# Kernel tuning notes

Hardware: AMD Instinct MI355X
Metric: run time of the kernel (lower is better)

The kernel has to match this reference:

```python
import jax, jax.numpy as jnp
import numpy as np

EMBED_DIM = 1024
NUM_HEADS = 16
HEAD_DIM = EMBED_DIM // NUM_HEADS


def setup_inputs() -> dict:
    key = jax.random.key(0)
    ks = jax.random.split(key, 12)
    B, S, E = 2, 2048, EMBED_DIM
    scale = 1.0 / np.sqrt(E)
    inp = {
        "query": jax.random.normal(ks[0], (B, S, E), dtype=jnp.float32),
        "key": jax.random.normal(ks[1], (B, S, E), dtype=jnp.float32),
        "value": jax.random.normal(ks[2], (B, S, E), dtype=jnp.float32),
        "key_padding_mask": jax.random.randint(ks[3], (B, S), 0, 2).astype(bool),
        # Linear params (torch nn.Linear: y = x @ W.T + b)
        "Wq": jax.random.normal(ks[4], (E, E), dtype=jnp.float32) * scale,
        "bq": jnp.zeros((E,), dtype=jnp.float32),
        "Wk": jax.random.normal(ks[5], (E, E), dtype=jnp.float32) * scale,
        "bk": jnp.zeros((E,), dtype=jnp.float32),
        "Wv": jax.random.normal(ks[6], (E, E), dtype=jnp.float32) * scale,
        "bv": jnp.zeros((E,), dtype=jnp.float32),
        "Wo": jax.random.normal(ks[7], (E, E), dtype=jnp.float32) * scale,
        "bo": jnp.zeros((E,), dtype=jnp.float32),
    }
    return inp


def reference(query, key, value, key_padding_mask, Wq, bq, Wk, bk, Wv, bv, Wo, bo):
    B, Sq, E = query.shape
    H, D = NUM_HEADS, HEAD_DIM

    def split_heads(x, W, b):
        y = x @ W.T + b                      # [B, S, E]
        return y.reshape(B, -1, H, D).transpose(0, 2, 1, 3)  # [B, H, S, D]

    q = split_heads(query, Wq, bq)
    k = split_heads(key, Wk, bk)
    v = split_heads(value, Wv, bv)

    scores = jnp.einsum("bhqd,bhkd->bhqk", q, k) / jnp.sqrt(jnp.float32(D))
    scores = jnp.where(key_padding_mask[:, None, None, :], -jnp.inf, scores)
    probs = jax.nn.softmax(scores, axis=-1)  # dropout p=0.0 -> identity
    attn = jnp.einsum("bhqk,bhkd->bhqd", probs, v)
    attn = attn.transpose(0, 2, 1, 3).reshape(B, Sq, E)
    return attn @ Wo.T + bo
```

## Files before the change

kernel.cpp:

```cpp
#include <hip/hip_runtime.h>
#include <hip/hip_bf16.h>

#define BATCH 2
#define SEQ   2048
#define EMBED 1024
#define NHEAD 16
#define HDIM  64

typedef __bf16 bf16x8 __attribute__((ext_vector_type(8)));
typedef __bf16 bf16x4 __attribute__((ext_vector_type(4)));
typedef float  floatx4 __attribute__((ext_vector_type(4)));

struct ConvAll { const void* src[7]; void* dst[7]; unsigned n[7]; };

__device__ __forceinline__ int derive_isbf(const void* qptr) {
    const unsigned short* u = (const unsigned short*)qptr;
    int sane = 0;
    for (int k = 0; k < 64; ++k) {
        int e = (u[2 * k] >> 7) & 0xff;
        if (e >= 117 && e <= 137) sane++;
    }
    return (sane >= 40) ? 1 : 0;
}

__global__ __launch_bounds__(256) void prep_convert(
        ConvAll a, const void* qptr, const void* mptr,
        int* flags, __hip_bfloat16* mones) {
    if (blockIdx.y == 7) {
        if (blockIdx.x >= 16) return;
        const unsigned int* w = (const unsigned int*)mptr;
        int all01 = 1, allf = 1;
        for (int i = 0; i < 64; ++i) {
            unsigned int x = w[i];
            if (!(x == 0u || x == 1u)) all01 = 0;
            if (!(x == 0u || x == 0x3F800000u)) allf = 0;
        }
        const int bytemask = (all01 || allf) ? 0 : 1;
        const int i = blockIdx.x * 256 + threadIdx.x;
        int v;
        if (bytemask) v = (((const unsigned char*)mptr)[i] != 0);
        else          v = (((const unsigned int*)mptr)[i] != 0u);
        mones[i] = __float2bfloat16(v ? 0.f : 1.f);
        if (blockIdx.x == 0 && threadIdx.x == 0) {
            flags[0] = derive_isbf(qptr);
            flags[1] = bytemask;
        }
        return;
    }
    if (derive_isbf(qptr)) return;
    const int t = blockIdx.y;
    const unsigned n8 = a.n[t] / 8;
    const unsigned stride = gridDim.x * blockDim.x;
    for (unsigned i = blockIdx.x * blockDim.x + threadIdx.x; i < n8; i += stride) {
        const unsigned base = i * 8;
        const float* s = (const float*)a.src[t] + base;
        __hip_bfloat16 tmp[8];
#pragma unroll
        for (int j = 0; j < 8; ++j) tmp[j] = __float2bfloat16(s[j]);
        *(uint4*)((__hip_bfloat16*)a.dst[t] + base) = *(const uint4*)tmp;
    }
}

__device__ __forceinline__ void gload_lds16(const __hip_bfloat16* g, __bf16* l) {
    __builtin_amdgcn_global_load_lds(
        (const __attribute__((address_space(1))) unsigned int*)g,
        (__attribute__((address_space(3))) unsigned int*)l, 16, 0, 0);
}

struct GemmIO {
    const void* Xr; const __hip_bfloat16* Xc;
    const void* Wr; const __hip_bfloat16* Wc;
    const void* br;
    void* Y;
    float osc;
};
struct GemmArgs { GemmIO io[3]; };

__global__ __launch_bounds__(256, 2) void gemm_mfma(
        GemmArgs args, int M, int N, int K, const int* flags,
        const __hip_bfloat16* __restrict__ mones) {
    const GemmIO io = args.io[blockIdx.z];
    const int isbf = flags[0];
    const __hip_bfloat16* Xp = isbf ? (const __hip_bfloat16*)io.Xr : io.Xc;
    const __hip_bfloat16* Wp = isbf ? (const __hip_bfloat16*)io.Wr : io.Wc;
    __shared__ __bf16 Xs[128 * 64];
    __shared__ __bf16 Ws[128 * 64];
    const int lane = threadIdx.x & 63, wv = threadIdx.x >> 6;
    const int wr = wv >> 1, wc = wv & 1;
    const int l = lane & 15, quad = lane >> 4;

    const int lin = blockIdx.x + blockIdx.y * 8;
    const int tsw = (lin & 7) * 32 + (lin >> 3);
    const int row0 = (tsw >> 3) * 128, col0 = (tsw & 7) * 128;

    const int srow = lane >> 3;
    const int schunk = (lane & 7) ^ srow;
    const __hip_bfloat16* xbase = Xp + (size_t)(row0 + srow) * K + schunk * 8;
    const __hip_bfloat16* wbase = Wp + (size_t)(col0 + srow) * K + schunk * 8;

    floatx4 acc[4][4] = {};

    for (int k0 = 0; k0 < K; k0 += 64) {
        __syncthreads();
#pragma unroll
        for (int i = 0; i < 4; ++i) {
            const int instr = wv * 4 + i;
            gload_lds16(xbase + (size_t)instr * 8 * K + k0, &Xs[instr * 512]);
        }
#pragma unroll
        for (int i = 0; i < 4; ++i) {
            const int instr = wv * 4 + i;
            gload_lds16(wbase + (size_t)instr * 8 * K + k0, &Ws[instr * 512]);
        }
        __syncthreads();
#pragma unroll
        for (int kk = 0; kk < 2; ++kk) {
            bf16x8 af[4], bfr[4];
#pragma unroll
            for (int m = 0; m < 4; ++m)
                af[m] = *(const bf16x8*)
                    &Xs[(wr * 64 + m * 16 + l) * 64 + ((kk * 4 + quad) ^ (l & 7)) * 8];
#pragma unroll
            for (int n = 0; n < 4; ++n)
                bfr[n] = *(const bf16x8*)
                    &Ws[(wc * 64 + n * 16 + l) * 64 + ((kk * 4 + quad) ^ (l & 7)) * 8];
#pragma unroll
            for (int m = 0; m < 4; ++m)
#pragma unroll
                for (int n = 0; n < 4; ++n)
                    acc[m][n] = __builtin_amdgcn_mfma_f32_16x16x32_bf16(
                        af[m], bfr[n], acc[m][n], 0, 0, 0);
        }
    }

    if (blockIdx.z == 2) {
#pragma unroll
        for (int m = 0; m < 4; ++m) {
            const int rb = row0 + wr * 64 + m * 16 + quad * 4;
            const int b = rb >> 11, s0 = rb & (SEQ - 1);
            float mf[4];
#pragma unroll
            for (int r = 0; r < 4; ++r)
                mf[r] = __bfloat162float(mones[rb + r]);
#pragma unroll
            for (int n = 0; n < 4; ++n) {
                const int col = col0 + wc * 64 + n * 16 + l;
                const int h = col >> 6, d = col & 63;
                const float bv = isbf
                    ? __bfloat162float(((const __hip_bfloat16*)io.br)[col])
                    : ((const float*)io.br)[col];
                bf16x4 out;
#pragma unroll
                for (int r = 0; r < 4; ++r)
                    out[r] = (__bf16)((acc[m][n][r] + bv) * mf[r]);
                *(bf16x4*)((__hip_bfloat16*)io.Y +
                           ((size_t)((b << 4) + h) * HDIM + d) * SEQ + s0) = out;
            }
        }
    } else {
#pragma unroll
        for (int m = 0; m < 4; ++m) {
#pragma unroll
            for (int n = 0; n < 4; ++n) {
                const int col = col0 + wc * 64 + n * 16 + l;
                const float bv = isbf
                    ? __bfloat162float(((const __hip_bfloat16*)io.br)[col])
                    : ((const float*)io.br)[col];
#pragma unroll
                for (int r = 0; r < 4; ++r) {
                    const int row = row0 + wr * 64 + m * 16 + quad * 4 + r;
                    const float v = (acc[m][n][r] + bv) * io.osc;
                    ((__hip_bfloat16*)io.Y)[(size_t)row * N + col] = __float2bfloat16(v);
                }
            }
        }
    }
}

__global__ __launch_bounds__(256, 2) void gemm_out(
        const __hip_bfloat16* __restrict__ X,
        const void* __restrict__ Wr, const __hip_bfloat16* __restrict__ Wc,
        const void* __restrict__ bias, void* __restrict__ Y,
        const int* flags) {
    const int N = EMBED, K = EMBED;
    const int isbf = flags[0];
    const __hip_bfloat16* Wp = isbf ? (const __hip_bfloat16*)Wr : Wc;
    __shared__ __bf16 Xs[64 * 64];
    __shared__ __bf16 Ws[128 * 64];
    const int lane = threadIdx.x & 63, wv = threadIdx.x >> 6;
    const int wr = wv >> 1, wc = wv & 1;
    const int l = lane & 15, quad = lane >> 4;

    const int lin = blockIdx.x + blockIdx.y * 8;
    const int tsw = (lin & 7) * 64 + (lin >> 3);
    const int row0 = (tsw >> 3) * 64, col0 = (tsw & 7) * 128;

    const int srow = lane >> 3;
    const int schunk = (lane & 7) ^ srow;
    const __hip_bfloat16* xbase = X + (size_t)(row0 + srow) * K + schunk * 8;
    const __hip_bfloat16* wbase = Wp + (size_t)(col0 + srow) * K + schunk * 8;

    floatx4 acc[2][4] = {};

    for (int k0 = 0; k0 < K; k0 += 64) {
        __syncthreads();
#pragma unroll
        for (int i = 0; i < 2; ++i) {
            const int instr = wv * 2 + i;
            gload_lds16(xbase + (size_t)instr * 8 * K + k0, &Xs[instr * 512]);
        }
#pragma unroll
        for (int i = 0; i < 4; ++i) {
            const int instr = wv * 4 + i;
            gload_lds16(wbase + (size_t)instr * 8 * K + k0, &Ws[instr * 512]);
        }
        __syncthreads();
#pragma unroll
        for (int kk = 0; kk < 2; ++kk) {
            bf16x8 af[2], bfr[4];
#pragma unroll
            for (int m = 0; m < 2; ++m)
                af[m] = *(const bf16x8*)
                    &Xs[(wr * 32 + m * 16 + l) * 64 + ((kk * 4 + quad) ^ (l & 7)) * 8];
#pragma unroll
            for (int n = 0; n < 4; ++n)
                bfr[n] = *(const bf16x8*)
                    &Ws[(wc * 64 + n * 16 + l) * 64 + ((kk * 4 + quad) ^ (l & 7)) * 8];
#pragma unroll
            for (int m = 0; m < 2; ++m)
#pragma unroll
                for (int n = 0; n < 4; ++n)
                    acc[m][n] = __builtin_amdgcn_mfma_f32_16x16x32_bf16(
                        af[m], bfr[n], acc[m][n], 0, 0, 0);
        }
    }

#pragma unroll
    for (int m = 0; m < 2; ++m) {
#pragma unroll
        for (int n = 0; n < 4; ++n) {
            const int col = col0 + wc * 64 + n * 16 + l;
            const float bv = isbf
                ? __bfloat162float(((const __hip_bfloat16*)bias)[col])
                : ((const float*)bias)[col];
#pragma unroll
            for (int r = 0; r < 4; ++r) {
                const int row = row0 + wr * 32 + m * 16 + quad * 4 + r;
                const float v = acc[m][n][r] + bv;
                if (isbf)
                    ((__hip_bfloat16*)Y)[(size_t)row * N + col] = __float2bfloat16(v);
                else
                    ((float*)Y)[(size_t)row * N + col] = v;
            }
        }
    }
}

__global__ __launch_bounds__(512, 4) void attn_mfma(
        const __hip_bfloat16* __restrict__ Qb,
        const __hip_bfloat16* __restrict__ Kb,
        const __hip_bfloat16* __restrict__ Vt,
        const __hip_bfloat16* __restrict__ mones,
        __hip_bfloat16* __restrict__ Ao) {
    const int bh = blockIdx.x, b = bh >> 4, h = bh & 15;
    const int q0 = blockIdx.y * 128;
    const int wv = threadIdx.x >> 6, lane = threadIdx.x & 63;
    const int l = lane & 15, quad = lane >> 4;

    __shared__ __bf16 Ks[2][128 * 64];
    __shared__ __bf16 Vs[2][64 * 128];

    bf16x8 aQ[2];
    {
        const int qrow = q0 + wv * 16 + l;
        const __hip_bfloat16* qp =
            Qb + ((size_t)(b * SEQ + qrow)) * EMBED + h * HDIM + quad * 8;
        aQ[0] = *(const bf16x8*)qp;
        aQ[1] = *(const bf16x8*)(qp + 32);
    }

    floatx4 O[4] = {};
    floatx4 Ol = {};
    const int rho = 8 * (l >> 2) + (l & 3);

    const int ksrow = lane >> 3, kpc = lane & 7;
    const int vsrow = lane >> 4, vpc = lane & 15;
    const __hip_bfloat16* mbase = mones + b * SEQ;

    auto stage = [&](int k0, int buf) {
#pragma unroll
        for (int i = 0; i < 2; ++i) {
            const int row = wv * 16 + i * 8 + ksrow;
            const int sc = kpc ^ ((row & 3) | (((row >> 3) & 1) << 2));
            gload_lds16(Kb + ((size_t)(b * SEQ + k0 + row)) * EMBED + h * HDIM +
                            sc * 8,
                        &Ks[buf][(wv * 16 + i * 8) * 64]);
        }
#pragma unroll
        for (int i = 0; i < 2; ++i) {
            const int row = wv * 8 + i * 4 + vsrow;
            const int sc = vpc ^ (row & 15);
            gload_lds16(Vt + ((size_t)(bh * HDIM + row)) * SEQ + k0 + sc * 8,
                        &Vs[buf][(wv * 8 + i * 4) * 128]);
        }
    };

    auto compute = [&](int k0, int buf) {
#pragma unroll
        for (int kh2 = 0; kh2 < 2; ++kh2) {
            bf16x8 a0[4], a1[4];
#pragma unroll
            for (int n = 0; n < 4; ++n) {
                const int rr = kh2 * 64 + 32 * (n >> 1) + 4 * (n & 1) + rho;
                const int f = (rr & 3) | (((rr >> 3) & 1) << 2);
                a0[n] = *(const bf16x8*)&Ks[buf][rr * 64 + ((quad) ^ f) * 8];
                a1[n] = *(const bf16x8*)&Ks[buf][rr * 64 + ((quad + 4) ^ f) * 8];
            }
            bf16x8 bv[2][4];
#pragma unroll
            for (int kh = 0; kh < 2; ++kh)
#pragma unroll
                for (int dt = 0; dt < 4; ++dt) {
                    const int c = kh2 * 8 + kh * 4 + quad;
                    bv[kh][dt] = *(const bf16x8*)
                        &Vs[buf][(dt * 16 + l) * 128 + (c ^ l) * 8];
                }
            bf16x8 vm[2];
#pragma unroll
            for (int kh = 0; kh < 2; ++kh)
                vm[kh] = *(const bf16x8*)
                    (mbase + k0 + kh2 * 64 + kh * 32 + quad * 8);

            floatx4 S[4];
            __builtin_amdgcn_s_setprio(1);
#pragma unroll
            for (int n = 0; n < 4; ++n) {
                floatx4 c = {};
                c = __builtin_amdgcn_mfma_f32_16x16x32_bf16(a0[n], aQ[0],
                                                            c, 0, 0, 0);
                c = __builtin_amdgcn_mfma_f32_16x16x32_bf16(a1[n], aQ[1],
                                                            c, 0, 0, 0);
                S[n] = c;
            }
            __builtin_amdgcn_s_setprio(0);
#pragma unroll
            for (int n = 0; n < 4; ++n)
#pragma unroll
                for (int r = 0; r < 4; ++r)
                    S[n][r] = __builtin_amdgcn_exp2f(S[n][r]);
#pragma unroll
            for (int kh = 0; kh < 2; ++kh) {
                bf16x8 ap;
#pragma unroll
                for (int j = 0; j < 4; ++j) {
                    ap[j]     = (__bf16)S[2 * kh][j];
                    ap[j + 4] = (__bf16)S[2 * kh + 1][j];
                }
                __builtin_amdgcn_s_setprio(1);
#pragma unroll
                for (int dt = 0; dt < 4; ++dt)
                    O[dt] = __builtin_amdgcn_mfma_f32_16x16x32_bf16(
                        ap, bv[kh][dt], O[dt], 0, 0, 0);
                Ol = __builtin_amdgcn_mfma_f32_16x16x32_bf16(
                    ap, vm[kh], Ol, 0, 0, 0);
                __builtin_amdgcn_s_setprio(0);
            }
        }
    };

    stage(0, 0);
    const int NT = SEQ / 128;
    for (int tt = 0; tt < NT; tt += 2) {
        __syncthreads();
        stage((tt + 1) * 128, 1);
        compute(tt * 128, 0);
        __syncthreads();
        if (tt + 2 < NT) stage((tt + 2) * 128, 0);
        compute((tt + 1) * 128, 1);
    }
#pragma unroll
    for (int r = 0; r < 4; ++r) {
        const float lr = Ol[r];
        const float inv = (lr > 0.f) ? __builtin_amdgcn_rcpf(lr) : 0.f;
        const int row = q0 + wv * 16 + quad * 4 + r;
#pragma unroll
        for (int dt = 0; dt < 4; ++dt)
            Ao[((size_t)(b * SEQ + row)) * EMBED + h * HDIM + dt * 16 + l] =
                __float2bfloat16(O[dt][r] * inv);
    }
}

extern "C" void kernel_launch(void* const* d_in, const int* in_sizes, int n_in,
                              void* d_out, int out_size, void* d_ws, size_t ws_size,
                              hipStream_t stream) {
    const void* query = d_in[0];
    const void* key   = d_in[1];
    const void* value = d_in[2];
    const void* mask  = d_in[3];

    char* ws = (char*)d_ws;
    int* flags = (int*)ws;
    __hip_bfloat16* mones = (__hip_bfloat16*)(ws + 2048);
    const size_t TEN = (size_t)BATCH * SEQ * EMBED;
    const size_t WEL = (size_t)EMBED * EMBED;
    char* p = ws + 32768;
    __hip_bfloat16* Qc  = (__hip_bfloat16*)p;  p += TEN * 2;
    __hip_bfloat16* Kc  = (__hip_bfloat16*)p;  p += TEN * 2;
    __hip_bfloat16* Vc  = (__hip_bfloat16*)p;  p += TEN * 2;
    __hip_bfloat16* Wqc = (__hip_bfloat16*)p;  p += WEL * 2;
    __hip_bfloat16* Wkc = (__hip_bfloat16*)p;  p += WEL * 2;
    __hip_bfloat16* Wvc = (__hip_bfloat16*)p;  p += WEL * 2;
    __hip_bfloat16* Woc = (__hip_bfloat16*)p;  p += WEL * 2;
    __hip_bfloat16* Qb  = (__hip_bfloat16*)p;  p += TEN * 2;
    __hip_bfloat16* Kb  = (__hip_bfloat16*)p;  p += TEN * 2;
    __hip_bfloat16* Vt  = (__hip_bfloat16*)p;  p += TEN * 2;
    __hip_bfloat16* Ao  = Qc;

    const int M = BATCH * SEQ;
    const float QSCALE = 0.125f * 1.44269504088896f;

    ConvAll ca;
    ca.src[0] = query;    ca.dst[0] = Qc;  ca.n[0] = (unsigned)TEN;
    ca.src[1] = key;      ca.dst[1] = Kc;  ca.n[1] = (unsigned)TEN;
    ca.src[2] = value;    ca.dst[2] = Vc;  ca.n[2] = (unsigned)TEN;
    ca.src[3] = d_in[4];  ca.dst[3] = Wqc; ca.n[3] = (unsigned)WEL;
    ca.src[4] = d_in[6];  ca.dst[4] = Wkc; ca.n[4] = (unsigned)WEL;
    ca.src[5] = d_in[8];  ca.dst[5] = Wvc; ca.n[5] = (unsigned)WEL;
    ca.src[6] = d_in[10]; ca.dst[6] = Woc; ca.n[6] = (unsigned)WEL;
    prep_convert<<<dim3(256, 8), 256, 0, stream>>>(ca, query, mask, flags, mones);

    GemmArgs qkv;
    qkv.io[0] = { query, Qc, d_in[4],  Wqc, d_in[5],  (void*)Qb, QSCALE };
    qkv.io[1] = { key,   Kc, d_in[6],  Wkc, d_in[7],  (void*)Kb, 1.0f };
    qkv.io[2] = { value, Vc, d_in[8],  Wvc, d_in[9],  (void*)Vt, 1.0f };
    gemm_mfma<<<dim3(EMBED / 128, M / 128, 3), 256, 0, stream>>>(
        qkv, M, EMBED, EMBED, flags, mones);

    attn_mfma<<<dim3(BATCH * NHEAD, SEQ / 128), 512, 0, stream>>>(
        Qb, Kb, Vt, mones, Ao);

    gemm_out<<<dim3(EMBED / 128, M / 64), 256, 0, stream>>>(
        Ao, d_in[10], Woc, d_in[11], d_out, flags);
}
```

Before: 215.2 us.

## Double-buffer LDS tiles in projection GEMMs to overlap loads with MFMA

Both GEMM kernels now split the 64-wide K tile into two 32-wide half tiles held in a two-slot LDS ring. The next half tile's global-to-LDS copy is issued before computing on the current one, so memory latency overlaps with MFMA work and the load barrier on the critical path goes away. The staging layout and XOR swizzle are reworked for 32-element rows. In exchange, each half-step does less MFMA work between barriers, and the async LDS writes rely on barrier ordering that may leave a race if the load instructions are not waited on.

Measured after the change: 223.1 us. 3.7% more time.

```diff
diff --git a/kernel.cpp b/kernel.cpp
--- a/kernel.cpp
+++ b/kernel.cpp
@@ -83,8 +83,8 @@
     const int isbf = flags[0];
     const __hip_bfloat16* Xp = isbf ? (const __hip_bfloat16*)io.Xr : io.Xc;
     const __hip_bfloat16* Wp = isbf ? (const __hip_bfloat16*)io.Wr : io.Wc;
-    __shared__ __bf16 Xs[128 * 64];
-    __shared__ __bf16 Ws[128 * 64];
+    __shared__ __bf16 Xs[2][128 * 32];
+    __shared__ __bf16 Ws[2][128 * 32];
     const int lane = threadIdx.x & 63, wv = threadIdx.x >> 6;
     const int wr = wv >> 1, wc = wv & 1;
     const int l = lane & 15, quad = lane >> 4;
@@ -93,44 +93,49 @@
     const int tsw = (lin & 7) * 32 + (lin >> 3);
     const int row0 = (tsw >> 3) * 128, col0 = (tsw & 7) * 128;
 
-    const int srow = lane >> 3;
-    const int schunk = (lane & 7) ^ srow;
-    const __hip_bfloat16* xbase = Xp + (size_t)(row0 + srow) * K + schunk * 8;
-    const __hip_bfloat16* wbase = Wp + (size_t)(col0 + srow) * K + schunk * 8;
+    const int srow4 = lane >> 2;
+    const int schunk = (lane & 3) ^ (srow4 & 3);
+    const __hip_bfloat16* xbase = Xp + (size_t)(row0 + wv * 16 + srow4) * K + schunk * 8;
+    const __hip_bfloat16* wbase = Wp + (size_t)(col0 + wv * 16 + srow4) * K + schunk * 8;
 
     floatx4 acc[4][4] = {};
 
+    auto stage = [&](int k0, int buf) {
+#pragma unroll
+        for (int i = 0; i < 2; ++i) {
+            gload_lds16(xbase + (size_t)i * 64 * K + k0,
+                        &Xs[buf][(i * 64 + wv * 16) * 32]);
+            gload_lds16(wbase + (size_t)i * 64 * K + k0,
+                        &Ws[buf][(i * 64 + wv * 16) * 32]);
+        }
+    };
+
+    auto compute = [&](int buf) {
+        bf16x8 af[4], bfr[4];
+#pragma unroll
+        for (int m = 0; m < 4; ++m)
+            af[m] = *(const bf16x8*)
+                &Xs[buf][(wr * 64 + m * 16 + l) * 32 + ((quad ^ (l & 3)) * 8)];
+#pragma unroll
+        for (int n = 0; n < 4; ++n)
+            bfr[n] = *(const bf16x8*)
+                &Ws[buf][(wc * 64 + n * 16 + l) * 32 + ((quad ^ (l & 3)) * 8)];
+#pragma unroll
+        for (int m = 0; m < 4; ++m)
+#pragma unroll
+            for (int n = 0; n < 4; ++n)
+                acc[m][n] = __builtin_amdgcn_mfma_f32_16x16x32_bf16(
+                    af[m], bfr[n], acc[m][n], 0, 0, 0);
+    };
+
+    stage(0, 0);
     for (int k0 = 0; k0 < K; k0 += 64) {
         __syncthreads();
-#pragma unroll
-        for (int i = 0; i < 4; ++i) {
-            const int instr = wv * 4 + i;
-            gload_lds16(xbase + (size_t)instr * 8 * K + k0, &Xs[instr * 512]);
-        }
-#pragma unroll
-        for (int i = 0; i < 4; ++i) {
-            const int instr = wv * 4 + i;
-            gload_lds16(wbase + (size_t)instr * 8 * K + k0, &Ws[instr * 512]);
-        }
-        __syncthreads();
-#pragma unroll
-        for (int kk = 0; kk < 2; ++kk) {
-            bf16x8 af[4], bfr[4];
-#pragma unroll
-            for (int m = 0; m < 4; ++m)
-                af[m] = *(const bf16x8*)
-                    &Xs[(wr * 64 + m * 16 + l) * 64 + ((kk * 4 + quad) ^ (l & 7)) * 8];
-#pragma unroll
-            for (int n = 0; n < 4; ++n)
-                bfr[n] = *(const bf16x8*)
-                    &Ws[(wc * 64 + n * 16 + l) * 64 + ((kk * 4 + quad) ^ (l & 7)) * 8];
-#pragma unroll
-            for (int m = 0; m < 4; ++m)
-#pragma unroll
-                for (int n = 0; n < 4; ++n)
-                    acc[m][n] = __builtin_amdgcn_mfma_f32_16x16x32_bf16(
-                        af[m], bfr[n], acc[m][n], 0, 0, 0);
-        }
+        stage(k0 + 32, 1);
+        compute(0);
+        __syncthreads();
+        if (k0 + 64 < K) stage(k0 + 64, 0);
+        compute(1);
     }
 
     if (blockIdx.z == 2) {
@@ -185,8 +190,8 @@
     const int N = EMBED, K = EMBED;
     const int isbf = flags[0];
     const __hip_bfloat16* Wp = isbf ? (const __hip_bfloat16*)Wr : Wc;
-    __shared__ __bf16 Xs[64 * 64];
-    __shared__ __bf16 Ws[128 * 64];
+    __shared__ __bf16 Xs[2][64 * 32];
+    __shared__ __bf16 Ws[2][128 * 32];
     const int lane = threadIdx.x & 63, wv = threadIdx.x >> 6;
     const int wr = wv >> 1, wc = wv & 1;
     const int l = lane & 15, quad = lane >> 4;
@@ -195,44 +200,47 @@
     const int tsw = (lin & 7) * 64 + (lin >> 3);
     const int row0 = (tsw >> 3) * 64, col0 = (tsw & 7) * 128;
 
-    const int srow = lane >> 3;
-    const int schunk = (lane & 7) ^ srow;
-    const __hip_bfloat16* xbase = X + (size_t)(row0 + srow) * K + schunk * 8;
-    const __hip_bfloat16* wbase = Wp + (size_t)(col0 + srow) * K + schunk * 8;
+    const int srow4 = lane >> 2;
+    const int schunk = (lane & 3) ^ (srow4 & 3);
+    const __hip_bfloat16* xbase = X + (size_t)(row0 + wv * 16 + srow4) * K + schunk * 8;
+    const __hip_bfloat16* wbase = Wp + (size_t)(col0 + wv * 16 + srow4) * K + schunk * 8;
 
     floatx4 acc[2][4] = {};
 
+    auto stage = [&](int k0, int buf) {
+        gload_lds16(xbase + k0, &Xs[buf][(wv * 16) * 32]);
+#pragma unroll
+        for (int i = 0; i < 2; ++i)
+            gload_lds16(wbase + (size_t)i * 64 * K + k0,
+                        &Ws[buf][(i * 64 + wv * 16) * 32]);
+    };
+
+    auto compute = [&](int buf) {
+        bf16x8 af[2], bfr[4];
+#pragma unroll
+        for (int m = 0; m < 2; ++m)
+            af[m] = *(const bf16x8*)
+                &Xs[buf][(wr * 32 + m * 16 + l) * 32 + ((quad ^ (l & 3)) * 8)];
+#pragma unroll
+        for (int n = 0; n < 4; ++n)
+            bfr[n] = *(const bf16x8*)
+                &Ws[buf][(wc * 64 + n * 16 + l) * 32 + ((quad ^ (l & 3)) * 8)];
+#pragma unroll
+        for (int m = 0; m < 2; ++m)
+#pragma unroll
+            for (int n = 0; n < 4; ++n)
+                acc[m][n] = __builtin_amdgcn_mfma_f32_16x16x32_bf16(
+                    af[m], bfr[n], acc[m][n], 0, 0, 0);
+    };
+
+    stage(0, 0);
     for (int k0 = 0; k0 < K; k0 += 64) {
         __syncthreads();
-#pragma unroll
-        for (int i = 0; i < 2; ++i) {
-            const int instr = wv * 2 + i;
-            gload_lds16(xbase + (size_t)instr * 8 * K + k0, &Xs[instr * 512]);
-        }
-#pragma unroll
-        for (int i = 0; i < 4; ++i) {
-            const int instr = wv * 4 + i;
-            gload_lds16(wbase + (size_t)instr * 8 * K + k0, &Ws[instr * 512]);
-        }
-        __syncthreads();
-#pragma unroll
-        for (int kk = 0; kk < 2; ++kk) {
-            bf16x8 af[2], bfr[4];
-#pragma unroll
-            for (int m = 0; m < 2; ++m)
-                af[m] = *(const bf16x8*)
-                    &Xs[(wr * 32 + m * 16 + l) * 64 + ((kk * 4 + quad) ^ (l & 7)) * 8];
-#pragma unroll
-            for (int n = 0; n < 4; ++n)
-                bfr[n] = *(const bf16x8*)
-                    &Ws[(wc * 64 + n * 16 + l) * 64 + ((kk * 4 + quad) ^ (l & 7)) * 8];
-#pragma unroll
-            for (int m = 0; m < 2; ++m)
-#pragma unroll
-                for (int n = 0; n < 4; ++n)
-                    acc[m][n] = __builtin_amdgcn_mfma_f32_16x16x32_bf16(
-                        af[m], bfr[n], acc[m][n], 0, 0, 0);
-        }
+        stage(k0 + 32, 1);
+        compute(0);
+        __syncthreads();
+        if (k0 + 64 < K) stage(k0 + 64, 0);
+        compute(1);
     }
 
 #pragma unroll
```
